# Kernel tuning notes

Measured on AMD Instinct MI355X. Metric: run time of the kernel, lower is better.

## Reference

```python
import jax, jax.numpy as jnp
import numpy as np

HEADS = 16
GROUPS = 4
C_IN = 1024
C_OUT = 1024


def att_linear(x, w, b):
    # x: [B,S,C_in], w: [G, C_in/G, C_out/G], b: [C_out]
    B, S, _ = x.shape
    xg = x.reshape(B, S, GROUPS, C_IN // GROUPS)
    out = jnp.einsum('bsgi,gio->bsgo', xg, w).reshape(B, S, C_OUT)
    return out + b


def restricted_softmax(score, margin=0.0):
    # clamp row max at 0, add exp(margin - max) margin term to denominator
    smax = jnp.maximum(jnp.max(score, axis=-1, keepdims=True), 0.0)
    e = jnp.exp(score - smax)
    return e / (jnp.sum(e, axis=-1, keepdims=True) + jnp.exp(margin - smax))


def setup_inputs() -> dict:
    key = jax.random.key(0)
    ks = jax.random.split(key, 9)
    B, S = 4, 1024
    dpg_in, dpg_out = C_IN // GROUPS, C_OUT // GROUPS
    wscale = 1.0 / np.sqrt(dpg_in)
    return {
        'query': jax.random.normal(ks[0], (B, S, C_IN), jnp.float32),
        'key': jax.random.normal(ks[1], (B, S, C_IN), jnp.float32),
        'value': jax.random.normal(ks[2], (B, S, C_IN), jnp.float32),
        'wq': jax.random.uniform(ks[3], (GROUPS, dpg_in, dpg_out), jnp.float32, -wscale, wscale),
        'bq': jax.random.uniform(ks[4], (C_OUT,), jnp.float32, -wscale, wscale),
        'wk': jax.random.uniform(ks[5], (GROUPS, dpg_in, dpg_out), jnp.float32, -wscale, wscale),
        'bk': jax.random.uniform(ks[6], (C_OUT,), jnp.float32, -wscale, wscale),
        'wv': jax.random.uniform(ks[7], (GROUPS, dpg_in, dpg_out), jnp.float32, -wscale, wscale),
        'bv': jax.random.uniform(ks[8], (C_OUT,), jnp.float32, -wscale, wscale),
    }


def reference(query, key, value, wq, bq, wk, bk, wv, bv):
    B, S, _ = query.shape
    d = C_OUT // HEADS
    q = att_linear(query, wq, bq).reshape(B, S, HEADS, d).transpose(0, 2, 1, 3)
    k = att_linear(key, wk, bk).reshape(B, S, HEADS, d).transpose(0, 2, 1, 3)
    v = att_linear(value, wv, bv).reshape(B, S, HEADS, d).transpose(0, 2, 1, 3)
    score = jnp.einsum('bhqd,bhkd->bhqk', q, k) / jnp.sqrt(jnp.float32(d))
    attn = restricted_softmax(score)  # dropout p=0
    out = jnp.einsum('bhqk,bhkd->bhqd', attn, v)
    return out.transpose(0, 2, 1, 3).reshape(B, S, C_OUT)
```

## Files before the change

kernel.cpp:

```cpp
#include <hip/hip_runtime.h>
#include <hip/hip_bf16.h>

#define HEADS   16
#define GROUPS  4
#define C_IN    1024
#define C_OUT   1024
#define BATCH   4
#define SEQ     1024
#define DHEAD   64
#define DPG     256
#define MROWS   (BATCH * SEQ)
#define NBH     (BATCH * HEADS)
#define W_ELEMS ((size_t)GROUPS * DPG * DPG)
#define N_ELEMS ((size_t)NBH * SEQ * DHEAD)

typedef short  bhalf8  __attribute__((ext_vector_type(8)));
typedef short  short4v __attribute__((ext_vector_type(4)));
typedef float  f32x4   __attribute__((ext_vector_type(4)));
typedef unsigned short ushort8v __attribute__((ext_vector_type(8)));

#define MFMA16 __builtin_amdgcn_mfma_f32_16x16x32_bf16

__device__ __forceinline__ unsigned short f2bf(float x) {
    union { __hip_bfloat16 b; unsigned short u; } c;
    c.b = __float2bfloat16(x);
    return c.u;
}
__device__ __forceinline__ float bf2f(unsigned short s) {
    return __uint_as_float(((unsigned int)s) << 16);
}

__device__ __forceinline__ void gload16(const void* gsrc, void* lds) {
    __builtin_amdgcn_global_load_lds(
        (const __attribute__((address_space(1))) unsigned int*)(unsigned long long)(uintptr_t)gsrc,
        (__attribute__((address_space(3))) unsigned int*)(unsigned int)(uintptr_t)lds,
        16, 0, 0);
}

__global__ void wsplit(const float* __restrict__ w0,
                       const float* __restrict__ w1,
                       const float* __restrict__ w2,
                       unsigned short* __restrict__ wtbase)
{
    const int tid = threadIdx.x;
    const int kt = blockIdx.x, ot = blockIdx.y;
    const int which = blockIdx.z >> 2, g = blockIdx.z & 3;
    const float* w = (which == 0) ? w0 : (which == 1) ? w1 : w2;
    unsigned short* wth = wtbase + (size_t)which * 2 * W_ELEMS;
    unsigned short* wtl = wth + W_ELEMS;

    __shared__ float Ls[64][68];
    const float* wg = w + (size_t)g * DPG * DPG;
#pragma unroll
    for (int p = 0; p < 4; ++p) {
        const int kk = 16 * p + (tid >> 4);
        const int oo = 4 * (tid & 15);
        const float4 v = *reinterpret_cast<const float4*>(
            wg + (size_t)(kt * 64 + kk) * DPG + ot * 64 + oo);
        Ls[kk][oo + 0] = v.x; Ls[kk][oo + 1] = v.y;
        Ls[kk][oo + 2] = v.z; Ls[kk][oo + 3] = v.w;
    }
    __syncthreads();
    unsigned short* th = wth + (size_t)g * DPG * DPG;
    unsigned short* tl = wtl + (size_t)g * DPG * DPG;
#pragma unroll
    for (int p = 0; p < 4; ++p) {
        const int oo = 16 * p + (tid >> 4);
        const int k4 = 4 * (tid & 15);
        ushort4 hv, lv;
        {
            float v0 = Ls[k4 + 0][oo], v1 = Ls[k4 + 1][oo];
            float v2 = Ls[k4 + 2][oo], v3 = Ls[k4 + 3][oo];
            hv.x = f2bf(v0); lv.x = f2bf(v0 - bf2f(hv.x));
            hv.y = f2bf(v1); lv.y = f2bf(v1 - bf2f(hv.y));
            hv.z = f2bf(v2); lv.z = f2bf(v2 - bf2f(hv.z));
            hv.w = f2bf(v3); lv.w = f2bf(v3 - bf2f(hv.w));
        }
        const size_t o = (size_t)(ot * 64 + oo) * DPG + kt * 64 + k4;
        *reinterpret_cast<ushort4*>(th + o) = hv;
        *reinterpret_cast<ushort4*>(tl + o) = lv;
    }
}

__launch_bounds__(256, 2)
__global__ void proj_mfma(const float* __restrict__ xq,
                          const float* __restrict__ xk,
                          const float* __restrict__ xv,
                          const unsigned short* __restrict__ wtbase,
                          const float* __restrict__ bq,
                          const float* __restrict__ bk,
                          const float* __restrict__ bv,
                          unsigned short* __restrict__ outbase)
{
    const int tid  = threadIdx.x;
    const int wave = tid >> 6;
    const int lane = tid & 63;
    const int h    = lane >> 4;
    const int ln   = lane & 15;
    const int mq   = wave >> 1;
    const int nq   = wave & 1;
    const int bx   = blockIdx.x;
    const int by   = blockIdx.y;
    const int which = blockIdx.z >> 2, g = blockIdx.z & 3;
    const int m0   = bx * 64;

    const float* x    = (which == 0) ? xq : (which == 1) ? xk : xv;
    const float* bias = (which == 0) ? bq : (which == 1) ? bk : bv;
    unsigned short* outh = outbase + (size_t)which * 2 * N_ELEMS;
    unsigned short* outl = outh + N_ELEMS;

    __shared__ uint4 smem4[3072];
    char* sp = (char*)smem4;

    f32x4 acc[2][4];
#pragma unroll
    for (int a = 0; a < 2; ++a)
#pragma unroll
        for (int b = 0; b < 4; ++b) acc[a][b] = (f32x4){0.f, 0.f, 0.f, 0.f};

    const float* xg = x + (size_t)m0 * C_IN + g * DPG;
    const unsigned short* wh = wtbase + (size_t)which * 2 * W_ELEMS
                             + ((size_t)g * DPG + by * 128) * DPG;
    const unsigned short* wl = wh + W_ELEMS;

    int b_goff[4], b_lds[4];
#pragma unroll
    for (int c = 0; c < 4; ++c) {
        const int o  = (c * 4 + wave) * 1024 + lane * 16;
        const int rw = o >> 7;
        const int kidx = ((o & 127) ^ ((rw & 7) << 4)) >> 1;
        b_goff[c] = rw * DPG + kidx;
        b_lds[c]  = (c * 4 + wave) * 1024;
    }

    const int arb = tid >> 4, ac = tid & 15;

    for (int it = 0; it < 4; ++it) {
        const int k0 = it * 64;
        if (it > 0) __syncthreads();
#pragma unroll
        for (int c = 0; c < 4; ++c) {
            gload16(wh + b_goff[c] + k0, sp + 16384 + b_lds[c]);
            gload16(wl + b_goff[c] + k0, sp + 32768 + b_lds[c]);
        }
#pragma unroll
        for (int p = 0; p < 4; ++p) {
            const int rr = 16 * p + arb;
            const float4 v = *reinterpret_cast<const float4*>(
                xg + (size_t)rr * C_IN + k0 + 4 * ac);
            ushort4 hv, lv;
            hv.x = f2bf(v.x); lv.x = f2bf(v.x - bf2f(hv.x));
            hv.y = f2bf(v.y); lv.y = f2bf(v.y - bf2f(hv.y));
            hv.z = f2bf(v.z); lv.z = f2bf(v.z - bf2f(hv.z));
            hv.w = f2bf(v.w); lv.w = f2bf(v.w - bf2f(hv.w));
            const int off = (8 * ac) ^ ((rr & 7) << 4);
            *reinterpret_cast<ushort4*>(sp + rr * 128 + off) = hv;
            *reinterpret_cast<ushort4*>(sp + 8192 + rr * 128 + off) = lv;
        }
        __syncthreads();

#pragma unroll
        for (int kk = 0; kk < 2; ++kk) {
            bhalf8 ah[2], al[2], bh_[4], bl_[4];
#pragma unroll
            for (int mt = 0; mt < 2; ++mt) {
                const int row = 32 * mq + 16 * mt + ln;
                const int off = (64 * kk + 16 * h) ^ ((row & 7) << 4);
                ah[mt] = *reinterpret_cast<const bhalf8*>(sp + row * 128 + off);
                al[mt] = *reinterpret_cast<const bhalf8*>(sp + 8192 + row * 128 + off);
            }
#pragma unroll
            for (int nt = 0; nt < 4; ++nt) {
                const int row = 64 * nq + 16 * nt + ln;
                const int off = (64 * kk + 16 * h) ^ ((row & 7) << 4);
                bh_[nt] = *reinterpret_cast<const bhalf8*>(sp + 16384 + row * 128 + off);
                bl_[nt] = *reinterpret_cast<const bhalf8*>(sp + 32768 + row * 128 + off);
            }
#pragma unroll
            for (int mt = 0; mt < 2; ++mt)
#pragma unroll
                for (int nt = 0; nt < 4; ++nt) {
                    acc[mt][nt] = MFMA16(ah[mt], bh_[nt], acc[mt][nt], 0, 0, 0);
                    acc[mt][nt] = MFMA16(al[mt], bh_[nt], acc[mt][nt], 0, 0, 0);
                    acc[mt][nt] = MFMA16(ah[mt], bl_[nt], acc[mt][nt], 0, 0, 0);
                }
        }
    }
    __syncthreads();

    const int hd = g * 4 + by * 2 + nq;
    const int b  = bx >> 4;
    const size_t bhb = ((size_t)b * HEADS + hd) * (SEQ * DHEAD);
    const int wbase = wave * 8192;
    const int sg0 = (bx & 15) * 64 + 32 * mq;
    const float oscale = (which == 0) ? 0.125f : 1.0f;
    float bnt[4];
#pragma unroll
    for (int nt = 0; nt < 4; ++nt)
        bnt[nt] = bias[g * 256 + by * 128 + 64 * nq + 16 * nt + ln];

    if (which != 2) {
#pragma unroll
        for (int mt = 0; mt < 2; ++mt)
#pragma unroll
            for (int nt = 0; nt < 4; ++nt)
#pragma unroll
                for (int r = 0; r < 4; ++r) {
                    const int sl = 16 * mt + 4 * h + r;
                    const float v = (acc[mt][nt][r] + bnt[nt]) * oscale;
                    const unsigned short hh = f2bf(v);
                    const unsigned short ll = f2bf(v - bf2f(hh));
                    const int cb = (2 * (16 * nt + ln)) ^ ((sl & 7) << 4);
                    *reinterpret_cast<unsigned short*>(sp + wbase + sl * 128 + cb) = hh;
                    *reinterpret_cast<unsigned short*>(sp + wbase + 4096 + sl * 128 + cb) = ll;
                }
        __syncthreads();
#pragma unroll
        for (int p = 0; p < 4; ++p) {
            const int sl = 8 * p + (lane >> 3);
            const int cb = (16 * (lane & 7)) ^ ((sl & 7) << 4);
            const size_t go = bhb + (size_t)(sg0 + sl) * 64 + 8 * (lane & 7);
            *reinterpret_cast<ushort8v*>(outh + go) =
                *reinterpret_cast<const ushort8v*>(sp + wbase + sl * 128 + cb);
            *reinterpret_cast<ushort8v*>(outl + go) =
                *reinterpret_cast<const ushort8v*>(sp + wbase + 4096 + sl * 128 + cb);
        }
    } else {
#pragma unroll
        for (int mt = 0; mt < 2; ++mt)
#pragma unroll
            for (int nt = 0; nt < 4; ++nt) {
                const int dl = 16 * nt + ln;
                ushort4 hv, lv;
                {
                    float v0 = acc[mt][nt][0] + bnt[nt];
                    float v1 = acc[mt][nt][1] + bnt[nt];
                    float v2 = acc[mt][nt][2] + bnt[nt];
                    float v3 = acc[mt][nt][3] + bnt[nt];
                    hv.x = f2bf(v0); lv.x = f2bf(v0 - bf2f(hv.x));
                    hv.y = f2bf(v1); lv.y = f2bf(v1 - bf2f(hv.y));
                    hv.z = f2bf(v2); lv.z = f2bf(v2 - bf2f(hv.z));
                    hv.w = f2bf(v3); lv.w = f2bf(v3 - bf2f(hv.w));
                }
                const int off = (32 * mt + 8 * h) ^ ((dl & 7) << 3);
                *reinterpret_cast<ushort4*>(sp + wbase + dl * 64 + off) = hv;
                *reinterpret_cast<ushort4*>(sp + wbase + 4096 + dl * 64 + off) = lv;
            }
        __syncthreads();
#pragma unroll
        for (int p = 0; p < 4; ++p) {
            const int dl  = 16 * p + (lane >> 2);
            const int c16 = 16 * (lane & 3);
            const int o0b = (c16) ^ ((dl & 7) << 3);
            const int o1b = (c16 + 8) ^ ((dl & 7) << 3);
            const size_t go = bhb + (size_t)dl * SEQ + sg0 + 8 * (lane & 3);
            *reinterpret_cast<ushort4*>(outh + go) =
                *reinterpret_cast<const ushort4*>(sp + wbase + dl * 64 + o0b);
            *reinterpret_cast<ushort4*>(outh + go + 4) =
                *reinterpret_cast<const ushort4*>(sp + wbase + dl * 64 + o1b);
            *reinterpret_cast<ushort4*>(outl + go) =
                *reinterpret_cast<const ushort4*>(sp + wbase + 4096 + dl * 64 + o0b);
            *reinterpret_cast<ushort4*>(outl + go + 4) =
                *reinterpret_cast<const ushort4*>(sp + wbase + 4096 + dl * 64 + o1b);
        }
    }
}

__launch_bounds__(256, 2)
__global__ void attn_mfma(const unsigned short* __restrict__ qh,
                          const unsigned short* __restrict__ ql,
                          const unsigned short* __restrict__ kh,
                          const unsigned short* __restrict__ kl,
                          const unsigned short* __restrict__ vth,
                          const unsigned short* __restrict__ vtl,
                          float* __restrict__ out)
{
    const int tid  = threadIdx.x;
    const int wave = tid >> 6;
    const int lane = tid & 63;
    const int h    = lane >> 4;
    const int ln   = lane & 15;
    const int bh   = blockIdx.x;
    const int q0   = blockIdx.y * 128 + wave * 32;

    const size_t bhbase = (size_t)bh * (SEQ * DHEAD);
    const unsigned short* qhp = qh + bhbase;
    const unsigned short* qlp = ql + bhbase;
    const unsigned short* khp = kh + bhbase;
    const unsigned short* klp = kl + bhbase;
    const unsigned short* vhp = vth + bhbase;
    const unsigned short* vlp = vtl + bhbase;

    __shared__ uint4 smem4[4096];
    char* sb = (char*)smem4;

    bhalf8 Qf[2][2][2];
#pragma unroll
    for (int nt = 0; nt < 2; ++nt)
#pragma unroll
        for (int dt = 0; dt < 2; ++dt) {
            const size_t o = (size_t)(q0 + 16 * nt + ln) * DHEAD + dt * 32 + 8 * h;
            Qf[nt][dt][0] = *reinterpret_cast<const bhalf8*>(qhp + o);
            Qf[nt][dt][1] = *reinterpret_cast<const bhalf8*>(qlp + o);
        }

    f32x4 accO[2][4];
#pragma unroll
    for (int a = 0; a < 2; ++a)
#pragma unroll
        for (int b = 0; b < 4; ++b) accO[a][b] = (f32x4){0.f, 0.f, 0.f, 0.f};
    float m_i[2] = {0.f, 0.f};
    float l_i[2] = {1.f, 1.f};

    int rw_[2], kd_[2], lofs_[2];
#pragma unroll
    for (int c = 0; c < 2; ++c) {
        const int o = (c * 4 + wave) * 1024 + lane * 16;
        rw_[c]   = o >> 7;
        kd_[c]   = ((o & 127) ^ ((rw_[c] & 7) << 4)) >> 1;
        lofs_[c] = (c * 4 + wave) * 1024;
    }

#define STAGE_TILE(BUF, K0)                                                        \
    do {                                                                           \
        _Pragma("unroll")                                                          \
        for (int c = 0; c < 2; ++c) {                                              \
            char* lb = sb + (BUF) + lofs_[c];                                      \
            const int rw = rw_[c], kd = kd_[c];                                    \
            gload16(khp + (size_t)((K0) + rw) * DHEAD + kd, lb);                   \
            gload16(klp + (size_t)((K0) + rw) * DHEAD + kd, lb + 8192);            \
            gload16(vhp + (size_t)rw * SEQ + (K0) + kd,     lb + 16384);           \
            gload16(vlp + (size_t)rw * SEQ + (K0) + kd,     lb + 24576);           \
        }                                                                          \
    } while (0)

    STAGE_TILE(0, 0);

    for (int t = 0; t < 16; ++t) {
        const int nb = ((t + 1) & 1) * 32768;
        const int nk = ((t + 1) & 15) * 64;
        STAGE_TILE(nb, nk);
        asm volatile("s_waitcnt vmcnt(8)\n\ts_barrier" ::: "memory");

        const char* cb = sb + (t & 1) * 32768;

        f32x4 s_[2][4];
#pragma unroll
        for (int a = 0; a < 2; ++a)
#pragma unroll
            for (int b = 0; b < 4; ++b) s_[a][b] = (f32x4){0.f, 0.f, 0.f, 0.f};
#pragma unroll
        for (int mt = 0; mt < 4; ++mt) {
            const int rr = 16 * mt + ln;
            const int sw = (rr & 7) << 4;
            const bhalf8 Ah0 = *reinterpret_cast<const bhalf8*>(cb + rr * 128 + ((16 * h) ^ sw));
            const bhalf8 Ah1 = *reinterpret_cast<const bhalf8*>(cb + rr * 128 + ((64 + 16 * h) ^ sw));
            const bhalf8 Al0 = *reinterpret_cast<const bhalf8*>(cb + 8192 + rr * 128 + ((16 * h) ^ sw));
            const bhalf8 Al1 = *reinterpret_cast<const bhalf8*>(cb + 8192 + rr * 128 + ((64 + 16 * h) ^ sw));
#pragma unroll
            for (int nt = 0; nt < 2; ++nt) {
                s_[nt][mt] = MFMA16(Ah0, Qf[nt][0][0], s_[nt][mt], 0, 0, 0);
                s_[nt][mt] = MFMA16(Ah1, Qf[nt][1][0], s_[nt][mt], 0, 0, 0);
                s_[nt][mt] = MFMA16(Ah0, Qf[nt][0][1], s_[nt][mt], 0, 0, 0);
                s_[nt][mt] = MFMA16(Ah1, Qf[nt][1][1], s_[nt][mt], 0, 0, 0);
                s_[nt][mt] = MFMA16(Al0, Qf[nt][0][0], s_[nt][mt], 0, 0, 0);
                s_[nt][mt] = MFMA16(Al1, Qf[nt][1][0], s_[nt][mt], 0, 0, 0);
            }
        }

        float Pv[2][4][4];
        bhalf8 Pfh[2][2], Pfl[2][2];
#pragma unroll
        for (int nt = 0; nt < 2; ++nt) {
            float mloc = -1e30f;
#pragma unroll
            for (int mt = 0; mt < 4; ++mt)
#pragma unroll
                for (int rr = 0; rr < 4; ++rr) {
                    const float v = s_[nt][mt][rr];
                    Pv[nt][mt][rr] = v;
                    mloc = fmaxf(mloc, v);
                }
            mloc = fmaxf(mloc, __shfl_xor(mloc, 16));
            mloc = fmaxf(mloc, __shfl_xor(mloc, 32));
            const float mn = fmaxf(m_i[nt], mloc);
            const float sf = __expf(m_i[nt] - mn);
            m_i[nt] = mn;
            float rs = 0.f;
#pragma unroll
            for (int mt = 0; mt < 4; ++mt)
#pragma unroll
                for (int rr = 0; rr < 4; ++rr) {
                    const float p = __expf(Pv[nt][mt][rr] - mn);
                    Pv[nt][mt][rr] = p;
                    rs += p;
                }
            rs += __shfl_xor(rs, 16);
            rs += __shfl_xor(rs, 32);
            l_i[nt] = l_i[nt] * sf + rs;
#pragma unroll
            for (int rr = 0; rr < 4; ++rr) {
                const float sf_b = __shfl(sf, 20 * h + rr);
#pragma unroll
                for (int ntd = 0; ntd < 4; ++ntd) accO[nt][ntd][rr] *= sf_b;
            }
#pragma unroll
            for (int kt = 0; kt < 2; ++kt) {
                bhalf8 fh, fl;
#pragma unroll
                for (int j = 0; j < 8; ++j) {
                    const float p = Pv[nt][2 * kt + (j >> 2)][j & 3];
                    const unsigned short hi = f2bf(p);
                    fh[j] = (short)hi;
                    fl[j] = (short)f2bf(p - bf2f(hi));
                }
                Pfh[nt][kt] = fh;
                Pfl[nt][kt] = fl;
            }
        }

#pragma unroll
        for (int kt = 0; kt < 2; ++kt) {
#pragma unroll
            for (int ntd = 0; ntd < 4; ++ntd) {
                const int rr = 16 * ntd + ln;
                const int sw = (rr & 7) << 4;
                const int c0 = (64 * kt + 8 * h) ^ sw;
                const int c1 = (64 * kt + 32 + 8 * h) ^ sw;
                union { short4v q[2]; bhalf8 v; } ubh, ubl;
                ubh.q[0] = *reinterpret_cast<const short4v*>(cb + 16384 + rr * 128 + c0);
                ubh.q[1] = *reinterpret_cast<const short4v*>(cb + 16384 + rr * 128 + c1);
                ubl.q[0] = *reinterpret_cast<const short4v*>(cb + 24576 + rr * 128 + c0);
                ubl.q[1] = *reinterpret_cast<const short4v*>(cb + 24576 + rr * 128 + c1);
                const bhalf8 Bh = ubh.v;
                const bhalf8 Bl = ubl.v;
#pragma unroll
                for (int nt = 0; nt < 2; ++nt) {
                    accO[nt][ntd] = MFMA16(Pfh[nt][kt], Bh, accO[nt][ntd], 0, 0, 0);
                    accO[nt][ntd] = MFMA16(Pfh[nt][kt], Bl, accO[nt][ntd], 0, 0, 0);
                    accO[nt][ntd] = MFMA16(Pfl[nt][kt], Bh, accO[nt][ntd], 0, 0, 0);
                }
            }
        }
        asm volatile("s_barrier" ::: "memory");
    }
    asm volatile("s_waitcnt vmcnt(0)" ::: "memory");

    const int bB = bh >> 4;
    const int hd = bh & 15;
#pragma unroll
    for (int nt = 0; nt < 2; ++nt) {
        float linv[4];
#pragma unroll
        for (int rr = 0; rr < 4; ++rr) linv[rr] = 1.0f / __shfl(l_i[nt], 20 * h + rr);
#pragma unroll
        for (int rr = 0; rr < 4; ++rr) {
            const int q = q0 + 16 * nt + 4 * h + rr;
            float* orow = out + ((size_t)bB * SEQ + q) * C_OUT + hd * DHEAD + ln;
#pragma unroll
            for (int ntd = 0; ntd < 4; ++ntd)
                orow[16 * ntd] = accO[nt][ntd][rr] * linv[rr];
        }
    }
#undef STAGE_TILE
}

extern "C" void kernel_launch(void* const* d_in, const int* in_sizes, int n_in,
                              void* d_out, int out_size, void* d_ws, size_t ws_size,
                              hipStream_t stream) {
    const float* query = (const float*)d_in[0];
    const float* key   = (const float*)d_in[1];
    const float* value = (const float*)d_in[2];
    const float* wq    = (const float*)d_in[3];
    const float* bq    = (const float*)d_in[4];
    const float* wk    = (const float*)d_in[5];
    const float* bk    = (const float*)d_in[6];
    const float* wv    = (const float*)d_in[7];
    const float* bv    = (const float*)d_in[8];

    unsigned short* qkv = (unsigned short*)d_ws;
    unsigned short* wts = qkv + 6 * N_ELEMS;

    dim3 blk(256);
    wsplit<<<dim3(4, 4, 12), blk, 0, stream>>>(wq, wk, wv, wts);
    proj_mfma<<<dim3(MROWS / 64, 2, 12), blk, 0, stream>>>(
        query, key, value, wts, bq, bk, bv, qkv);

    attn_mfma<<<dim3(NBH, SEQ / 128), blk, 0, stream>>>(
        qkv, qkv + N_ELEMS, qkv + 2 * N_ELEMS, qkv + 3 * N_ELEMS,
        qkv + 4 * N_ELEMS, qkv + 5 * N_ELEMS, (float*)d_out);
}
```

Baseline: 191.7 us.

## Single-buffer V tile, raise occupancy, use exp2 with lazy rescale in attention

V is no longer double-buffered. Only K tiles are double-buffered, and V is loaded into one shared buffer behind an extra mid-iteration barrier, so LDS per block drops from 64KB to 48KB. That reduction allows three blocks per CU instead of two. The Q projection folds log2(e) into its scale so the softmax can use raw v_exp_f32 (exp2). The online-softmax rescale of the accumulator now runs only when the running max grows by more than a threshold, which skips most rescale work but adds a barrier and a serialised V load.

```diff
diff --git a/kernel.cpp b/kernel.cpp
--- a/kernel.cpp
+++ b/kernel.cpp
@@ -28,6 +28,11 @@
 }
 __device__ __forceinline__ float bf2f(unsigned short s) {
     return __uint_as_float(((unsigned int)s) << 16);
+}
+__device__ __forceinline__ float exp2a(float x) {
+    float r;
+    asm("v_exp_f32 %0, %1" : "=v"(r) : "v"(x));
+    return r;
 }
 
 __device__ __forceinline__ void gload16(const void* gsrc, void* lds) {
@@ -193,7 +198,7 @@
     const size_t bhb = ((size_t)b * HEADS + hd) * (SEQ * DHEAD);
     const int wbase = wave * 8192;
     const int sg0 = (bx & 15) * 64 + 32 * mq;
-    const float oscale = (which == 0) ? 0.125f : 1.0f;
+    const float oscale = (which == 0) ? 0.18033688011112042f : 1.0f;
     float bnt[4];
 #pragma unroll
     for (int nt = 0; nt < 4; ++nt)
@@ -266,7 +271,7 @@
     }
 }
 
-__launch_bounds__(256, 2)
+__launch_bounds__(256, 3)
 __global__ void attn_mfma(const unsigned short* __restrict__ qh,
                           const unsigned short* __restrict__ ql,
                           const unsigned short* __restrict__ kh,
@@ -291,7 +296,7 @@
     const unsigned short* vhp = vth + bhbase;
     const unsigned short* vlp = vtl + bhbase;
 
-    __shared__ uint4 smem4[4096];
+    __shared__ uint4 smem4[3072];
     char* sb = (char*)smem4;
 
     bhalf8 Qf[2][2][2];
@@ -321,28 +326,33 @@
         lofs_[c] = (c * 4 + wave) * 1024;
     }
 
-#define STAGE_TILE(BUF, K0)                                                        \
-    do {                                                                           \
-        _Pragma("unroll")                                                          \
-        for (int c = 0; c < 2; ++c) {                                              \
-            char* lb = sb + (BUF) + lofs_[c];                                      \
-            const int rw = rw_[c], kd = kd_[c];                                    \
-            gload16(khp + (size_t)((K0) + rw) * DHEAD + kd, lb);                   \
-            gload16(klp + (size_t)((K0) + rw) * DHEAD + kd, lb + 8192);            \
-            gload16(vhp + (size_t)rw * SEQ + (K0) + kd,     lb + 16384);           \
-            gload16(vlp + (size_t)rw * SEQ + (K0) + kd,     lb + 24576);           \
-        }                                                                          \
+#define STAGE_K(BUF, K0)                                                       \
+    do {                                                                       \
+        _Pragma("unroll")                                                      \
+        for (int c = 0; c < 2; ++c) {                                          \
+            char* lb = sb + (BUF) + lofs_[c];                                  \
+            gload16(khp + (size_t)((K0) + rw_[c]) * DHEAD + kd_[c], lb);       \
+            gload16(klp + (size_t)((K0) + rw_[c]) * DHEAD + kd_[c], lb + 8192);\
+        }                                                                      \
     } while (0)
-
-    STAGE_TILE(0, 0);
+#define STAGE_V(K0)                                                            \
+    do {                                                                       \
+        _Pragma("unroll")                                                      \
+        for (int c = 0; c < 2; ++c) {                                          \
+            char* lb = sb + 32768 + lofs_[c];                                  \
+            gload16(vhp + (size_t)rw_[c] * SEQ + (K0) + kd_[c], lb);           \
+            gload16(vlp + (size_t)rw_[c] * SEQ + (K0) + kd_[c], lb + 8192);    \
+        }                                                                      \
+    } while (0)
+
+    STAGE_K(0, 0);
 
     for (int t = 0; t < 16; ++t) {
-        const int nb = ((t + 1) & 1) * 32768;
-        const int nk = ((t + 1) & 15) * 64;
-        STAGE_TILE(nb, nk);
+        STAGE_V(t * 64);
+        STAGE_K(((t + 1) & 1) * 16384, ((t + 1) & 15) * 64);
         asm volatile("s_waitcnt vmcnt(8)\n\ts_barrier" ::: "memory");
 
-        const char* cb = sb + (t & 1) * 32768;
+        const char* cb = sb + (t & 1) * 16384;
 
         f32x4 s_[2][4];
 #pragma unroll
@@ -383,27 +393,31 @@
                 }
             mloc = fmaxf(mloc, __shfl_xor(mloc, 16));
             mloc = fmaxf(mloc, __shfl_xor(mloc, 32));
-            const float mn = fmaxf(m_i[nt], mloc);
-            const float sf = __expf(m_i[nt] - mn);
-            m_i[nt] = mn;
+            if (__any(mloc > m_i[nt] + 10.0f)) {
+                const float mn = fmaxf(m_i[nt], mloc);
+                const float sf = exp2a(m_i[nt] - mn);
+                m_i[nt] = mn;
+                l_i[nt] *= sf;
+#pragma unroll
+                for (int rr = 0; rr < 4; ++rr) {
+                    const float sf_b = __shfl(sf, 20 * h + rr);
+#pragma unroll
+                    for (int ntd = 0; ntd < 4; ++ntd) accO[nt][ntd][rr] *= sf_b;
+                }
+            }
             float rs = 0.f;
+            const float mcur = m_i[nt];
 #pragma unroll
             for (int mt = 0; mt < 4; ++mt)
 #pragma unroll
                 for (int rr = 0; rr < 4; ++rr) {
-                    const float p = __expf(Pv[nt][mt][rr] - mn);
+                    const float p = exp2a(Pv[nt][mt][rr] - mcur);
                     Pv[nt][mt][rr] = p;
                     rs += p;
                 }
             rs += __shfl_xor(rs, 16);
             rs += __shfl_xor(rs, 32);
-            l_i[nt] = l_i[nt] * sf + rs;
-#pragma unroll
-            for (int rr = 0; rr < 4; ++rr) {
-                const float sf_b = __shfl(sf, 20 * h + rr);
-#pragma unroll
-                for (int ntd = 0; ntd < 4; ++ntd) accO[nt][ntd][rr] *= sf_b;
-            }
+            l_i[nt] += rs;
 #pragma unroll
             for (int kt = 0; kt < 2; ++kt) {
                 bhalf8 fh, fl;
@@ -418,6 +432,8 @@
                 Pfl[nt][kt] = fl;
             }
         }
+
+        asm volatile("s_waitcnt vmcnt(4)\n\ts_barrier" ::: "memory");
 
 #pragma unroll
         for (int kt = 0; kt < 2; ++kt) {
@@ -428,10 +444,10 @@
                 const int c0 = (64 * kt + 8 * h) ^ sw;
                 const int c1 = (64 * kt + 32 + 8 * h) ^ sw;
                 union { short4v q[2]; bhalf8 v; } ubh, ubl;
-                ubh.q[0] = *reinterpret_cast<const short4v*>(cb + 16384 + rr * 128 + c0);
-                ubh.q[1] = *reinterpret_cast<const short4v*>(cb + 16384 + rr * 128 + c1);
-                ubl.q[0] = *reinterpret_cast<const short4v*>(cb + 24576 + rr * 128 + c0);
-                ubl.q[1] = *reinterpret_cast<const short4v*>(cb + 24576 + rr * 128 + c1);
+                ubh.q[0] = *reinterpret_cast<const short4v*>(sb + 32768 + rr * 128 + c0);
+                ubh.q[1] = *reinterpret_cast<const short4v*>(sb + 32768 + rr * 128 + c1);
+                ubl.q[0] = *reinterpret_cast<const short4v*>(sb + 40960 + rr * 128 + c0);
+                ubl.q[1] = *reinterpret_cast<const short4v*>(sb + 40960 + rr * 128 + c1);
                 const bhalf8 Bh = ubh.v;
                 const bhalf8 Bl = ubl.v;
 #pragma unroll
@@ -462,7 +478,8 @@
                 orow[16 * ntd] = accO[nt][ntd][rr] * linv[rr];
         }
     }
-#undef STAGE_TILE
+#undef STAGE_K
+#undef STAGE_V
 }
 
 extern "C" void kernel_launch(void* const* d_in, const int* in_sizes, int n_in,
```

Result: faster. 182.8 us (-4.7%).
